# Kernel tuning notes

Measured on AMD Instinct MI355X. Metric: run time of the kernel, lower is better.

Reference implementation:

```python
import jax, jax.numpy as jnp
import numpy as np
from jax import lax

B, S, T = 16, 256, 800
V, D, M, H = 256, 512, 80, 1024
NH = 4; HD = D // NH; EH = 256  # encoder LSTM hidden per direction


def setup_inputs() -> dict:
    key = jax.random.key(0)
    it = iter(jax.random.split(key, 40))
    def rn(shape, s=0.05):
        return jax.random.normal(next(it), shape, jnp.float32) * s
    return dict(
        text_inputs=jax.random.randint(next(it), (B, S), 0, V),
        mel_targets=jax.random.normal(next(it), (B, T, M), jnp.float32),
        emb=rn((V, D), 0.1),
        conv_w=rn((3, D, D, 5)), conv_b=rn((3, D)),
        bn_gamma=jnp.ones((3, D)), bn_beta=jnp.zeros((3, D)),
        bn_mean=rn((3, D)), bn_var=jnp.ones((3, D)),
        enc_Wih_f=rn((4 * EH, D)), enc_Whh_f=rn((4 * EH, EH)), enc_b_f=rn((4 * EH,)),
        enc_Wih_b=rn((4 * EH, D)), enc_Whh_b=rn((4 * EH, EH)), enc_b_b=rn((4 * EH,)),
        Wq=rn((D, M)), bq=rn((D,)), Wk=rn((D, D)), bk=rn((D,)),
        Wv=rn((D, D)), bv=rn((D,)), Wo=rn((D, D)), bo=rn((D,)),
        dec_Wih1=rn((4 * H, D + M)), dec_b1=rn((4 * H,)),
        dec_Wih2=rn((4 * H, H)), dec_b2=rn((4 * H,)),
        mel_W=rn((M, H)), mel_b=rn((M,)),
        stop_W=rn((1, H)), stop_b=rn((1,)),
    )


def _lstm_cell_zero(x, Wih, b):
    # single-step LSTM cell from zero (h, c); original resets state every timestep
    g = x @ Wih.T + b
    i, f, gg, o = jnp.split(g, 4, axis=-1)
    c = jax.nn.sigmoid(i) * jnp.tanh(gg)  # c0 = 0 -> forget gate contributes nothing
    return jax.nn.sigmoid(o) * jnp.tanh(c)


def _lstm_scan(xs, Wih, Whh, b, hdim, reverse):
    # xs: (S, B, in); PyTorch gate order i,f,g,o
    def step(carry, xt):
        h, c = carry
        g = xt @ Wih.T + h @ Whh.T + b
        i, f, gg, o = jnp.split(g, 4, axis=-1)
        c = jax.nn.sigmoid(f) * c + jax.nn.sigmoid(i) * jnp.tanh(gg)
        h = jax.nn.sigmoid(o) * jnp.tanh(c)
        return (h, c), h
    z = jnp.zeros((xs.shape[1], hdim), xs.dtype)
    _, hs = lax.scan(step, (z, z), xs, reverse=reverse)
    return hs


def reference(text_inputs, mel_targets, emb, conv_w, conv_b, bn_gamma, bn_beta, bn_mean, bn_var, enc_Wih_f, enc_Whh_f, enc_b_f, enc_Wih_b, enc_Whh_b, enc_b_b, Wq, bq, Wk, bk, Wv, bv, Wo, bo, dec_Wih1, dec_b1, dec_Wih2, dec_b2, mel_W, mel_b, stop_W, stop_b):
    b_, t_, m_ = mel_targets.shape
    # ---- encoder ----
    x = emb[text_inputs].transpose(0, 2, 1)  # (B, D, S)
    for i in range(conv_w.shape[0]):
        x = lax.conv_general_dilated(x, conv_w[i], (1,), [(2, 2)], dimension_numbers=('NCH', 'OIH', 'NCH')) + conv_b[i][None, :, None]
        x = bn_gamma[i][None, :, None] * (x - bn_mean[i][None, :, None]) * lax.rsqrt(bn_var[i][None, :, None] + 1e-5) + bn_beta[i][None, :, None]
        x = jax.nn.relu(x)  # dropout in eval mode -> identity
    xs = x.transpose(2, 0, 1)  # (S, B, D)
    hf = _lstm_scan(xs, enc_Wih_f, enc_Whh_f, enc_b_f, EH, False)
    hb = _lstm_scan(xs, enc_Wih_b, enc_Whh_b, enc_b_b, EH, True)
    enc = jnp.concatenate([hf, hb], -1).transpose(1, 0, 2)  # (B, S, D)
    # ---- decoder (teacher forcing): per-step query = previous mel frame ----
    dec_in = jnp.concatenate([jnp.zeros((b_, 1, m_), mel_targets.dtype), mel_targets[:, :-1]], axis=1)  # (B, T, M)
    q = (dec_in @ Wq.T + bq).reshape(b_, t_, NH, HD)
    k = (enc @ Wk.T + bk).reshape(b_, -1, NH, HD)
    v = (enc @ Wv.T + bv).reshape(b_, -1, NH, HD)
    scores = jnp.einsum('bqhd,bkhd->bhqk', q, k) * (1.0 / np.sqrt(HD)).astype(np.float32)
    attn = jax.nn.softmax(scores, axis=-1)
    ctx = jnp.einsum('bhqk,bkhd->bqhd', attn, v).reshape(b_, t_, D) @ Wo.T + bo
    xcat = jnp.concatenate([ctx, dec_in], axis=-1)  # (B, T, D+M)
    # original re-inits decoder LSTM state each timestep -> stateless per-step cells
    h1 = _lstm_cell_zero(xcat, dec_Wih1, dec_b1)
    h2 = _lstm_cell_zero(h1, dec_Wih2, dec_b2)
    mel = h2 @ mel_W.T + mel_b      # (B, T, 80)
    stop = h2 @ stop_W.T + stop_b   # (B, T, 1) - logits (no sigmoid in training path)
    return mel, stop
```

## Files before the change

### kernel.cpp

```cpp
#include <hip/hip_runtime.h>
#include <hip/hip_bf16.h>
#include <math.h>

#define B_ 16
#define S_ 256
#define T_ 800
#define V_ 256
#define D_ 512
#define M_ 80
#define H_ 1024
#define NH_ 4
#define HD_ 128
#define EH_ 256

using bf16x8 = __attribute__((ext_vector_type(8))) short;
using f32x4  = __attribute__((ext_vector_type(4))) float;
typedef _Float16 half8 __attribute__((ext_vector_type(8)));

__device__ __forceinline__ float sigf(float x) { return 1.f / (1.f + __expf(-x)); }
__device__ __forceinline__ float tanhfast(float x) {
    float e = __expf(2.f * x);
    return 1.f - 2.f / (e + 1.f);
}

__device__ __forceinline__ unsigned short f2bf(float f) {
    unsigned int u = __float_as_uint(f);
    unsigned int r = (u + 0x7FFFu + ((u >> 16) & 1u)) >> 16;
    return (unsigned short)r;
}
__device__ __forceinline__ float bf2f(unsigned short u) {
    return __uint_as_float(((unsigned int)u) << 16);
}
__device__ __forceinline__ unsigned short h2u(_Float16 x) {
    union { _Float16 f; unsigned short u; } c; c.f = x; return c.u;
}

__device__ __forceinline__ void gl_lds16(const unsigned short* g, unsigned short* l) {
    __builtin_amdgcn_global_load_lds((const __attribute__((address_space(1))) void*)g,
                                     (__attribute__((address_space(3))) void*)l, 16, 0, 0);
}

__global__ __launch_bounds__(256) void gemm_mfma(
    const unsigned short* __restrict__ A, const unsigned short* __restrict__ Bw,
    void* __restrict__ Cv, const float* __restrict__ bias,
    int M, int N, int K, int ldc, int epi, int aperm,
    const float* __restrict__ cb)
{
    __shared__ unsigned short As[4096];
    __shared__ unsigned short Bs[4096];
    const int tid = threadIdx.x, w = tid >> 6, lane = tid & 63;
    const int bm = blockIdx.y * 128, bn = blockIdx.x * 128;
    const int wr = w >> 1, wc = w & 1;

    f32x4 acc[4][4];
#pragma unroll
    for (int m = 0; m < 4; ++m)
#pragma unroll
        for (int n = 0; n < 4; ++n) acc[m][n] = (f32x4){0.f, 0.f, 0.f, 0.f};

    const int r0 = w * 16 + (lane >> 2);
    const int k8 = (lane & 3) * 8;
    int ar0 = bm + r0, ar1 = bm + r0 + 64;
    if (aperm) {
        ar0 = ((ar0 & 15) << 8) | (ar0 >> 4);
        ar1 = ((ar1 & 15) << 8) | (ar1 >> 4);
    }
    const unsigned short* Ag0 = A + (size_t)ar0 * K + k8;
    const unsigned short* Ag1 = A + (size_t)ar1 * K + k8;
    const unsigned short* Bg = Bw + (size_t)(bn + r0) * K + k8;
    unsigned short* Al = As + w * 512;
    unsigned short* Bl = Bs + w * 512;

    for (int k0 = 0; k0 < K; k0 += 32) {
        __syncthreads();
        gl_lds16(Ag0 + k0, Al);
        gl_lds16(Ag1 + k0, Al + 2048);
        gl_lds16(Bg + k0, Bl);
        gl_lds16(Bg + (size_t)64 * K + k0, Bl + 2048);
        __syncthreads();
        bf16x8 a[4], b[4];
#pragma unroll
        for (int m = 0; m < 4; ++m)
            a[m] = *(const bf16x8*)(As + (wr * 64 + m * 16 + (lane & 15)) * 32 + (lane >> 4) * 8);
#pragma unroll
        for (int n = 0; n < 4; ++n)
            b[n] = *(const bf16x8*)(Bs + (wc * 64 + n * 16 + (lane & 15)) * 32 + (lane >> 4) * 8);
#pragma unroll
        for (int m = 0; m < 4; ++m)
#pragma unroll
            for (int n = 0; n < 4; ++n)
                acc[m][n] = __builtin_amdgcn_mfma_f32_16x16x32_bf16(a[m], b[n], acc[m][n], 0, 0, 0);
    }

    const int cr = (lane >> 4) * 4, ccol = lane & 15;
#pragma unroll
    for (int m = 0; m < 4; ++m)
#pragma unroll
        for (int n = 0; n < 4; ++n) {
            const int col = bn + wc * 64 + n * 16 + ccol;
            float bv;
            if (epi == 5)      bv = (col < 512) ? bias[col] : cb[col - 512];
            else if (epi == 4) bv = (col < 80) ? bias[col] : (col == 80 ? cb[0] : 0.f);
            else               bv = bias ? bias[col] : 0.f;
#pragma unroll
            for (int j = 0; j < 4; ++j) {
                const int row = bm + wr * 64 + m * 16 + cr + j;
                float v = acc[m][n][j] + bv;
                if (epi == 2) {
                    ((unsigned short*)Cv)[(size_t)row * ldc + col] = f2bf(v);
                } else if (epi == 5) {
                    if (col < 512) {
                        ((unsigned short*)Cv)[(size_t)row * 512 + col] = f2bf(v);
                    } else {
                        unsigned short* vTo = (unsigned short*)Cv + 2097152;
                        const int c2 = col - 512, hh = c2 >> 7, dd = c2 & 127;
                        const int bb2 = row >> 8, ss = row & 255;
                        vTo[((size_t)(bb2 * 4 + hh) * 128 + dd) * 256 + ss] = f2bf(v);
                    }
                } else if (epi == 4) {
                    if (col < 80)       ((float*)Cv)[(size_t)row * ldc + col] = v;
                    else if (col == 80) ((float*)Cv)[1024000 + row] = v;
                } else {
                    ((float*)Cv)[(size_t)row * ldc + col] = v;
                }
            }
        }
}

__global__ __launch_bounds__(256) void conv_mfma(
    const unsigned short* __restrict__ xin, const unsigned short* __restrict__ Bw,
    unsigned short* __restrict__ xout,
    const float* __restrict__ cb, const float* __restrict__ gam,
    const float* __restrict__ bet, const float* __restrict__ mu,
    const float* __restrict__ va, const unsigned short* __restrict__ zbuf)
{
    __shared__ unsigned short As[4096];
    __shared__ unsigned short Bs[4096];
    const int tid = threadIdx.x, w = tid >> 6, lane = tid & 63;
    const int bm = blockIdx.y * 128, bn = blockIdx.x * 128;
    const int wr = w >> 1, wc = w & 1;

    f32x4 acc[4][4];
#pragma unroll
    for (int m = 0; m < 4; ++m)
#pragma unroll
        for (int n = 0; n < 4; ++n) acc[m][n] = (f32x4){0.f, 0.f, 0.f, 0.f};

    const int r0 = w * 16 + (lane >> 2);
    const int k8 = (lane & 3) * 8;
    const int gr0 = bm + r0, gr1 = bm + r0 + 64;
    const int b0 = gr0 >> 8, s0 = gr0 & 255;
    const int b1 = gr1 >> 8, s1 = gr1 & 255;
    const unsigned short* Bg = Bw + (size_t)(bn + r0) * 2560 + k8;
    unsigned short* Al = As + w * 512;
    unsigned short* Bl = Bs + w * 512;

    for (int k0 = 0; k0 < 2560; k0 += 32) {
        const int kk = k0 >> 9;
        const int d0 = k0 & 511;
        const int s2a = s0 + kk - 2;
        const int s2b = s1 + kk - 2;
        const unsigned short* pa = (s2a >= 0 && s2a < 256)
            ? xin + ((size_t)(b0 * 256 + s2a) * 512 + d0 + k8) : zbuf;
        const unsigned short* pb = (s2b >= 0 && s2b < 256)
            ? xin + ((size_t)(b1 * 256 + s2b) * 512 + d0 + k8) : zbuf;
        __syncthreads();
        gl_lds16(pa, Al);
        gl_lds16(pb, Al + 2048);
        gl_lds16(Bg + k0, Bl);
        gl_lds16(Bg + (size_t)64 * 2560 + k0, Bl + 2048);
        __syncthreads();
        bf16x8 a[4], b[4];
#pragma unroll
        for (int m = 0; m < 4; ++m)
            a[m] = *(const bf16x8*)(As + (wr * 64 + m * 16 + (lane & 15)) * 32 + (lane >> 4) * 8);
#pragma unroll
        for (int n = 0; n < 4; ++n)
            b[n] = *(const bf16x8*)(Bs + (wc * 64 + n * 16 + (lane & 15)) * 32 + (lane >> 4) * 8);
#pragma unroll
        for (int m = 0; m < 4; ++m)
#pragma unroll
            for (int n = 0; n < 4; ++n)
                acc[m][n] = __builtin_amdgcn_mfma_f32_16x16x32_bf16(a[m], b[n], acc[m][n], 0, 0, 0);
    }

    const int cr = (lane >> 4) * 4, ccol = lane & 15;
#pragma unroll
    for (int m = 0; m < 4; ++m)
#pragma unroll
        for (int n = 0; n < 4; ++n) {
            const int col = bn + wc * 64 + n * 16 + ccol;
            const float bc = cb[col], gm = gam[col], bt = bet[col];
            const float mv = mu[col], iv = rsqrtf(va[col] + 1e-5f);
#pragma unroll
            for (int j = 0; j < 4; ++j) {
                const int row = bm + wr * 64 + m * 16 + cr + j;
                float x = acc[m][n][j] + bc;
                float y = fmaxf(0.f, gm * (x - mv) * iv + bt);
                xout[(size_t)row * 512 + col] = f2bf(y);
            }
        }
}

__global__ __launch_bounds__(256) void attn_qksm(
    const unsigned short* __restrict__ q, const unsigned short* __restrict__ k,
    unsigned short* __restrict__ probs)
{
    __shared__ unsigned short As[2048];
    __shared__ unsigned short Bs[8192];
    __shared__ float redm[64][4];
    __shared__ float reds[64][4];
    const int tid = threadIdx.x, wid = tid >> 6, lane = tid & 63;
    const int l15 = lane & 15, bq = lane >> 4;
    const int bm = blockIdx.x * 64;
    const int z = blockIdx.y, b = z >> 2, h = z & 3;

    const unsigned short* A  = q + ((size_t)b * T_) * 512 + h * 128;
    const unsigned short* Bw = k + ((size_t)b * S_) * 512 + h * 128;

    f32x4 acc[4][4];
#pragma unroll
    for (int m = 0; m < 4; ++m)
#pragma unroll
        for (int n = 0; n < 4; ++n) acc[m][n] = (f32x4){0.f, 0.f, 0.f, 0.f};

    const int r0 = wid * 16 + (lane >> 2);
    const int k8 = (lane & 3) * 8;

    for (int k0 = 0; k0 < 128; k0 += 32) {
        __syncthreads();
        gl_lds16(A + (size_t)(bm + r0) * 512 + k0 + k8, As + wid * 512);
        gl_lds16(Bw + (size_t)r0 * 512 + k0 + k8,          Bs + wid * 512);
        gl_lds16(Bw + (size_t)(64 + r0) * 512 + k0 + k8,   Bs + 2048 + wid * 512);
        gl_lds16(Bw + (size_t)(128 + r0) * 512 + k0 + k8,  Bs + 4096 + wid * 512);
        gl_lds16(Bw + (size_t)(192 + r0) * 512 + k0 + k8,  Bs + 6144 + wid * 512);
        __syncthreads();
        bf16x8 a[4], bb[4];
#pragma unroll
        for (int m = 0; m < 4; ++m)
            a[m] = *(const bf16x8*)(As + (m * 16 + l15) * 32 + bq * 8);
#pragma unroll
        for (int n = 0; n < 4; ++n)
            bb[n] = *(const bf16x8*)(Bs + (wid * 64 + n * 16 + l15) * 32 + bq * 8);
#pragma unroll
        for (int m = 0; m < 4; ++m)
#pragma unroll
            for (int n = 0; n < 4; ++n)
                acc[m][n] = __builtin_amdgcn_mfma_f32_16x16x32_bf16(a[m], bb[n], acc[m][n], 0, 0, 0);
    }

    const int cr = (lane >> 4) * 4, ccol = lane & 15;
    const float SC = 0.08838834764831843f;

#pragma unroll
    for (int m = 0; m < 4; ++m)
#pragma unroll
        for (int j = 0; j < 4; ++j) {
            float v = fmaxf(fmaxf(acc[m][0][j], acc[m][1][j]),
                            fmaxf(acc[m][2][j], acc[m][3][j]));
#pragma unroll
            for (int off = 1; off < 16; off <<= 1) v = fmaxf(v, __shfl_xor(v, off));
            if (ccol == 0) redm[m * 16 + cr + j][wid] = v;
        }
    __syncthreads();
#pragma unroll
    for (int m = 0; m < 4; ++m)
#pragma unroll
        for (int j = 0; j < 4; ++j) {
            const int r = m * 16 + cr + j;
            float mx = fmaxf(fmaxf(redm[r][0], redm[r][1]), fmaxf(redm[r][2], redm[r][3]));
            float s = 0.f;
#pragma unroll
            for (int n = 0; n < 4; ++n) {
                float p = __expf((acc[m][n][j] - mx) * SC);
                acc[m][n][j] = p;
                s += p;
            }
#pragma unroll
            for (int off = 1; off < 16; off <<= 1) s += __shfl_xor(s, off);
            if (ccol == 0) reds[r][wid] = s;
        }
    __syncthreads();
#pragma unroll
    for (int m = 0; m < 4; ++m)
#pragma unroll
        for (int j = 0; j < 4; ++j) {
            const int r = m * 16 + cr + j;
            const int row = bm + r;
            if (row >= T_) continue;
            const float inv = 1.f / (reds[r][0] + reds[r][1] + reds[r][2] + reds[r][3]);
#pragma unroll
            for (int n = 0; n < 4; ++n)
                probs[((size_t)z * T_ + row) * 256 + wid * 64 + n * 16 + ccol] =
                    f2bf(acc[m][n][j] * inv);
        }
}

__global__ __launch_bounds__(256) void attn_pv(
    const unsigned short* __restrict__ probs, const unsigned short* __restrict__ vT,
    unsigned short* __restrict__ ctx)
{
    __shared__ unsigned short As[4096];
    __shared__ unsigned short Bs[4096];
    const int tid = threadIdx.x, w = tid >> 6, lane = tid & 63;
    const int bm = blockIdx.y * 128;
    const int z = blockIdx.z, b = z >> 2, h = z & 3;
    const int wr = w >> 1, wc = w & 1;

    const unsigned short* A  = probs + (size_t)z * T_ * 256;
    const unsigned short* Bw = vT + (size_t)z * 128 * 256;

    f32x4 acc[4][4];
#pragma unroll
    for (int m = 0; m < 4; ++m)
#pragma unroll
        for (int n = 0; n < 4; ++n) acc[m][n] = (f32x4){0.f, 0.f, 0.f, 0.f};

    const int r0 = w * 16 + (lane >> 2);
    const int k8 = (lane & 3) * 8;
    const unsigned short* Ag = A + (size_t)(bm + r0) * 256 + k8;
    const unsigned short* Bg = Bw + (size_t)r0 * 256 + k8;
    unsigned short* Al = As + w * 512;
    unsigned short* Bl = Bs + w * 512;

    for (int k0 = 0; k0 < 256; k0 += 32) {
        __syncthreads();
        gl_lds16(Ag + k0, Al);
        gl_lds16(Ag + (size_t)64 * 256 + k0, Al + 2048);
        gl_lds16(Bg + k0, Bl);
        gl_lds16(Bg + (size_t)64 * 256 + k0, Bl + 2048);
        __syncthreads();
        bf16x8 a[4], bfr[4];
#pragma unroll
        for (int m = 0; m < 4; ++m)
            a[m] = *(const bf16x8*)(As + (wr * 64 + m * 16 + (lane & 15)) * 32 + (lane >> 4) * 8);
#pragma unroll
        for (int n = 0; n < 4; ++n)
            bfr[n] = *(const bf16x8*)(Bs + (wc * 64 + n * 16 + (lane & 15)) * 32 + (lane >> 4) * 8);
#pragma unroll
        for (int m = 0; m < 4; ++m)
#pragma unroll
            for (int n = 0; n < 4; ++n)
                acc[m][n] = __builtin_amdgcn_mfma_f32_16x16x32_bf16(a[m], bfr[n], acc[m][n], 0, 0, 0);
    }

    const int cr = (lane >> 4) * 4, ccol = lane & 15;
#pragma unroll
    for (int m = 0; m < 4; ++m)
#pragma unroll
        for (int n = 0; n < 4; ++n) {
            const int col = wc * 64 + n * 16 + ccol;
#pragma unroll
            for (int j = 0; j < 4; ++j) {
                const int row = bm + wr * 64 + m * 16 + cr + j;
                if (row < T_)
                    ctx[((size_t)b * T_ + row) * 512 + h * 128 + col] = f2bf(acc[m][n][j]);
            }
        }
}

__global__ void hist2enc(const _Float16* __restrict__ hist, unsigned short* __restrict__ enc)
{
    int idx = blockIdx.x * 256 + threadIdx.x;
    if (idx >= B_ * S_ * D_) return;
    int d = idx & 511;
    int bs = idx >> 9;
    int b = bs >> 8, s = bs & 255;
    int dir = d >> 8, hid = d & 255;
    enc[idx] = f2bf((float)hist[(((size_t)(dir * 16 + b) * 256 + s) * 256) + hid]);
}

__global__ void cvt_all(
    const float* __restrict__ conv_w, const float* __restrict__ Wih_f,
    const float* __restrict__ Wih_b, const float* __restrict__ Wk,
    const float* __restrict__ Wv, const float* __restrict__ Wq,
    const float* __restrict__ Wo, const float* __restrict__ Wih1,
    const float* __restrict__ Wih2, const float* __restrict__ melW,
    const float* __restrict__ stopW,
    const int* __restrict__ txt, const float* __restrict__ emb,
    const float* __restrict__ mel,
    unsigned short* __restrict__ cWc, unsigned short* __restrict__ cWif,
    unsigned short* __restrict__ cWib, unsigned short* __restrict__ cWkv,
    unsigned short* __restrict__ cWq, unsigned short* __restrict__ cWo,
    unsigned short* __restrict__ cW1, unsigned short* __restrict__ cW2,
    unsigned short* __restrict__ cWm,
    unsigned short* __restrict__ xb0, unsigned short* __restrict__ din,
    unsigned short* __restrict__ xcat)
{
    int idx = blockIdx.x * 256 + threadIdx.x;
    if (idx < 3932160) {
        int n = idx / 2560, c = idx - n * 2560;
        int kk = c >> 9, din2 = c & 511;
        cWc[idx] = f2bf(conv_w[(size_t)n * 2560 + din2 * 5 + kk]);
        return;
    }
    idx -= 3932160;
    if (idx < 524288) { cWif[idx] = f2bf(Wih_f[idx]); return; }
    idx -= 524288;
    if (idx < 524288) { cWib[idx] = f2bf(Wih_b[idx]); return; }
    idx -= 524288;
    if (idx < 524288) {
        int r = idx >> 9, k = idx & 511;
        cWkv[idx] = (r < 512) ? f2bf(Wk[(size_t)r * 512 + k])
                              : f2bf(Wv[(size_t)(r - 512) * 512 + k]);
        return;
    }
    idx -= 524288;
    if (idx < 49152) {
        int r = idx / 96, k = idx - r * 96;
        cWq[idx] = (k < 80) ? f2bf(Wq[(size_t)r * 80 + k]) : 0;
        return;
    }
    idx -= 49152;
    if (idx < 262144) { cWo[idx] = f2bf(Wo[idx]); return; }
    idx -= 262144;
    if (idx < 1867776) {
        int n = idx / 608, k = idx - n * 608;
        int orig = (n < 1024) ? n : n + 1024;
        cW1[idx] = (k < 592) ? f2bf(Wih1[(size_t)orig * 592 + k]) : 0;
        return;
    }
    idx -= 1867776;
    if (idx < 3145728) {
        int n = idx >> 10, k = idx & 1023;
        int orig = (n < 1024) ? n : n + 1024;
        cW2[idx] = f2bf(Wih2[(size_t)orig * 1024 + k]);
        return;
    }
    idx -= 3145728;
    if (idx < 131072) {
        int r = idx >> 10, k = idx & 1023;
        cWm[idx] = (r < 80) ? f2bf(melW[(size_t)r * 1024 + k])
                            : (r == 80 ? f2bf(stopW[k]) : 0);
        return;
    }
    idx -= 131072;
    if (idx < B_ * S_ * D_) {
        int bs = idx >> 9, dd = idx & 511;
        xb0[idx] = f2bf(emb[(size_t)txt[bs] * D_ + dd]);
        return;
    }
    idx -= B_ * S_ * D_;
    if (idx < B_ * T_ * 96) {
        int r = idx / 96, j = idx - r * 96;
        int b = r / T_, t = r - b * T_;
        float v = (j < M_ && t > 0) ? mel[((size_t)b * T_ + t - 1) * M_ + j] : 0.f;
        unsigned short bv = f2bf(v);
        din[(size_t)r * 96 + j] = bv;
        xcat[(size_t)r * 608 + 512 + j] = bv;
        return;
    }
}

__global__ void dec_cellb2(const unsigned short* __restrict__ g, const float* __restrict__ b,
                           unsigned short* __restrict__ h, int rows)
{
    int idx = blockIdx.x * 256 + threadIdx.x;
    if (idx >= rows * 512) return;
    int r = idx >> 9, j2 = (idx & 511) * 2;
    const unsigned short* gr = g + (size_t)r * 3072;
    ushort2 vi = *(const ushort2*)(gr + j2);
    ushort2 vg = *(const ushort2*)(gr + 1024 + j2);
    ushort2 vo = *(const ushort2*)(gr + 2048 + j2);
    float i0 = sigf(bf2f(vi.x) + b[j2]),          i1 = sigf(bf2f(vi.y) + b[j2 + 1]);
    float g0 = tanhfast(bf2f(vg.x) + b[2048 + j2]), g1 = tanhfast(bf2f(vg.y) + b[2048 + j2 + 1]);
    float o0 = sigf(bf2f(vo.x) + b[3072 + j2]),   o1 = sigf(bf2f(vo.y) + b[3072 + j2 + 1]);
    ushort2 o;
    o.x = f2bf(o0 * tanhfast(i0 * g0));
    o.y = f2bf(o1 * tanhfast(i1 * g1));
    *(ushort2*)(h + (size_t)r * 1024 + j2) = o;
}

__global__ __launch_bounds__(1024, 4) void lstm_persist9(
    const float* __restrict__ gi_f, const float* __restrict__ gi_b,
    const float* __restrict__ Wf, const float* __restrict__ Wb,
    _Float16* __restrict__ hist,
    unsigned long long* __restrict__ hstage)
{
    const int blk = blockIdx.x;
    const int dir = blk >> 1, half = blk & 1;
    const float* gi = dir ? gi_b : gi_f;
    const float* W  = dir ? Wb : Wf;
    const int tid = threadIdx.x, wid = tid >> 6, lane = tid & 63;
    const int l15 = lane & 15, q = lane >> 4;
    const int half4 = half * 4, ph4 = (half ^ 1) * 4;

    __shared__ _Float16 h_lds[16][264];
    __shared__ float exch[512][17];

    half8 wOA[4], wPA[4], wOB[4], wPB[4];
    {
        const int gt0 = wid >> 3, hb0 = wid & 7;
        const int gt1 = (wid + 16) >> 3;
        const float* wr0 = W + (size_t)(gt0 * 256 + half * 128 + hb0 * 16 + l15) * 256;
        const float* wr1 = W + (size_t)(gt1 * 256 + half * 128 + hb0 * 16 + l15) * 256;
#pragma unroll
        for (int i = 0; i < 4; ++i) {
            const int kO = (half4 + i) * 32 + q * 8;
            const int kP = (ph4 + i) * 32 + q * 8;
            half8 a, b, c, d;
#pragma unroll
            for (int j = 0; j < 8; ++j) {
                a[j] = (_Float16)wr0[kO + j];
                b[j] = (_Float16)wr0[kP + j];
                c[j] = (_Float16)wr1[kO + j];
                d[j] = (_Float16)wr1[kP + j];
            }
            wOA[i] = a; wPA[i] = b; wOB[i] = c; wPB[i] = d;
        }
    }
    for (int i = tid; i < 16 * 264; i += 1024) ((_Float16*)h_lds)[i] = (_Float16)0.f;
    for (int i = tid; i < 512 * 17; i += 1024) ((float*)exch)[i] = 0.f;

    const int hid = tid & 127;
    const int ba  = tid >> 7;
    const int bb  = ba + 8;
    const int gh  = half * 128 + hid;
    const int pc  = (half ^ 1) * 128 + hid;
    float c0 = 0.f, c1 = 0.f;

    const int exr0 = (wid >> 3) * 128 + (wid & 7) * 16 + l15;
    const int exr1 = ((wid + 16) >> 3) * 128 + (wid & 7) * 16 + l15;

    const int own_base = ((dir * 2 + half) * 8 + ba) * 128 + hid;
    const int par_base = ((dir * 2 + (half ^ 1)) * 8 + ba) * 128 + hid;

    float gp0[4], gp1[4];
    {
        const int s0 = dir ? 255 : 0;
        const float* g0 = gi + ((size_t)s0 * 16 + ba) * 1024 + gh;
        const float* g1 = gi + ((size_t)s0 * 16 + bb) * 1024 + gh;
#pragma unroll
        for (int g2 = 0; g2 < 4; ++g2) { gp0[g2] = g0[g2 * 256]; gp1[g2] = g1[g2 * 256]; }
    }
    __syncthreads();

    for (int step = 0; step < 256; ++step) {
        const int s = dir ? (255 - step) : step;
        const unsigned int tag = (unsigned int)(step + 1);
        const int slot = (step & 1) * 4096;

        float h0, h1;
        {
            float xi = exch[hid][ba] + gp0[0];
            float xf = exch[128 + hid][ba] + gp0[1];
            float xg = exch[256 + hid][ba] + gp0[2];
            float xo = exch[384 + hid][ba] + gp0[3];
            float ig = sigf(xi), fg = sigf(xf), gg = tanhfast(xg), og = sigf(xo);
            c0 = fg * c0 + ig * gg; h0 = og * tanhfast(c0);
            xi = exch[hid][bb] + gp1[0];
            xf = exch[128 + hid][bb] + gp1[1];
            xg = exch[256 + hid][bb] + gp1[2];
            xo = exch[384 + hid][bb] + gp1[3];
            ig = sigf(xi); fg = sigf(xf); gg = tanhfast(xg); og = sigf(xo);
            c1 = fg * c1 + ig * gg; h1 = og * tanhfast(c1);
        }
        {
            unsigned int d32 = (unsigned int)h2u((_Float16)h0) |
                               ((unsigned int)h2u((_Float16)h1) << 16);
            unsigned long long wv = ((unsigned long long)tag << 32) | d32;
            __hip_atomic_store(&hstage[slot + own_base], wv,
                               __ATOMIC_RELAXED, __HIP_MEMORY_SCOPE_AGENT);
        }
        h_lds[ba][gh] = (_Float16)h0;
        h_lds[bb][gh] = (_Float16)h1;
        hist[(((size_t)(dir * 16 + ba) * 256 + s) * 256) + gh] = (_Float16)h0;
        hist[(((size_t)(dir * 16 + bb) * 256 + s) * 256) + gh] = (_Float16)h1;
        if (step < 255) {
            const int s2 = dir ? (254 - step) : (step + 1);
            const float* g0 = gi + ((size_t)s2 * 16 + ba) * 1024 + gh;
            const float* g1 = gi + ((size_t)s2 * 16 + bb) * 1024 + gh;
#pragma unroll
            for (int g2 = 0; g2 < 4; ++g2) { gp0[g2] = g0[g2 * 256]; gp1[g2] = g1[g2 * 256]; }
        }
        __syncthreads();

        if (step < 255) {
            f32x4 acc0 = (f32x4){0.f, 0.f, 0.f, 0.f};
            f32x4 acc1 = (f32x4){0.f, 0.f, 0.f, 0.f};
            const _Float16* hrow = &h_lds[l15][0];
#pragma unroll
            for (int i = 0; i < 4; ++i) {
                half8 a = *(const half8*)(hrow + (half4 + i) * 32 + q * 8);
                acc0 = __builtin_amdgcn_mfma_f32_16x16x32_f16(a, wOA[i], acc0, 0, 0, 0);
                acc1 = __builtin_amdgcn_mfma_f32_16x16x32_f16(a, wOB[i], acc1, 0, 0, 0);
            }
            {
                unsigned long long pv;
                do {
                    pv = __hip_atomic_load(&hstage[slot + par_base],
                                           __ATOMIC_RELAXED, __HIP_MEMORY_SCOPE_AGENT);
                } while ((unsigned int)(pv >> 32) != tag);
                unsigned int d32 = (unsigned int)pv;
                *(unsigned short*)&h_lds[ba][pc] = (unsigned short)(d32 & 0xFFFF);
                *(unsigned short*)&h_lds[bb][pc] = (unsigned short)(d32 >> 16);
            }
            __syncthreads();
#pragma unroll
            for (int i = 0; i < 4; ++i) {
                half8 a = *(const half8*)(hrow + (ph4 + i) * 32 + q * 8);
                acc0 = __builtin_amdgcn_mfma_f32_16x16x32_f16(a, wPA[i], acc0, 0, 0, 0);
                acc1 = __builtin_amdgcn_mfma_f32_16x16x32_f16(a, wPB[i], acc1, 0, 0, 0);
            }
            *(f32x4*)&exch[exr0][q * 4] = acc0;
            *(f32x4*)&exch[exr1][q * 4] = acc1;
            __syncthreads();
        }
    }
}

static inline void launch_mfma(hipStream_t st, const unsigned short* A, const unsigned short* B,
                               void* C, const float* bias, int M, int N, int K, int ldc,
                               int epi = 0, int aperm = 0, const float* cb = nullptr)
{
    dim3 grid(N / 128, M / 128);
    gemm_mfma<<<grid, 256, 0, st>>>(A, B, C, bias, M, N, K, ldc, epi, aperm, cb);
}

extern "C" void kernel_launch(void* const* d_in, const int* in_sizes, int n_in,
                              void* d_out, int out_size, void* d_ws, size_t ws_size,
                              hipStream_t stream)
{
    const int*   text   = (const int*)d_in[0];
    const float* mel_t  = (const float*)d_in[1];
    const float* emb    = (const float*)d_in[2];
    const float* conv_w = (const float*)d_in[3];
    const float* conv_b = (const float*)d_in[4];
    const float* bn_g   = (const float*)d_in[5];
    const float* bn_b   = (const float*)d_in[6];
    const float* bn_m   = (const float*)d_in[7];
    const float* bn_v   = (const float*)d_in[8];
    const float* Wih_f  = (const float*)d_in[9];
    const float* Whh_f  = (const float*)d_in[10];
    const float* b_f    = (const float*)d_in[11];
    const float* Wih_b  = (const float*)d_in[12];
    const float* Whh_b  = (const float*)d_in[13];
    const float* b_b    = (const float*)d_in[14];
    const float* Wq     = (const float*)d_in[15];
    const float* bq     = (const float*)d_in[16];
    const float* Wk     = (const float*)d_in[17];
    const float* bk     = (const float*)d_in[18];
    const float* Wv     = (const float*)d_in[19];
    const float* bv     = (const float*)d_in[20];
    const float* Wo     = (const float*)d_in[21];
    const float* bo     = (const float*)d_in[22];
    const float* Wih1   = (const float*)d_in[23];
    const float* b1     = (const float*)d_in[24];
    const float* Wih2   = (const float*)d_in[25];
    const float* b2     = (const float*)d_in[26];
    const float* melW   = (const float*)d_in[27];
    const float* melb   = (const float*)d_in[28];
    const float* stopW  = (const float*)d_in[29];
    const float* stopb  = (const float*)d_in[30];
    float* out = (float*)d_out;
    (void)in_sizes; (void)n_in; (void)out_size; (void)ws_size;

    float* ws = (float*)d_ws;
    float* big  = ws;
    float* pool = ws + 13107200;

    unsigned long long* hstage = (unsigned long long*)(ws + 6000000);
    const unsigned short* zbuf = (const unsigned short*)(hstage + 8192);

    float*          gi_f   = pool + 0;
    float*          gi_b   = pool + 4194304;
    unsigned short* enc_bf = (unsigned short*)(pool + 8388608);
    unsigned short* xb0    = (unsigned short*)(pool + 9437184);
    unsigned short* xb1    = (unsigned short*)(pool + 10485760);
    unsigned short* xb2    = (unsigned short*)(pool + 11534336);
    unsigned short* xb3    = (unsigned short*)(pool + 12582912);
    _Float16*       hist   = (_Float16*)(pool + 14155776);
    unsigned short* kbf    = (unsigned short*)(pool + 0);
    unsigned short* vT     = (unsigned short*)(pool + 1048576);
    unsigned short* qbf    = (unsigned short*)(pool + 2097152);
    unsigned short* probs  = (unsigned short*)(pool + 9437184);
    unsigned short* dinb   = (unsigned short*)(pool + 16008192);
    unsigned short* ctxb   = (unsigned short*)(pool + 16622592);
    unsigned short* gatesb = (unsigned short*)(pool + 0);
    unsigned short* h2b    = (unsigned short*)big;
    unsigned short* h1b    = (unsigned short*)(big + 4000000);
    unsigned short* xcat   = (unsigned short*)(pool + 19899392);
    float*          WB     = pool + 23790592;
    unsigned short* cWc  = (unsigned short*)(WB + 0);
    unsigned short* cWif = (unsigned short*)(WB + 1966080);
    unsigned short* cWib = (unsigned short*)(WB + 2228224);
    unsigned short* cWkv = (unsigned short*)(WB + 2490368);
    unsigned short* cWq  = (unsigned short*)(WB + 2752512);
    unsigned short* cWo  = (unsigned short*)(WB + 2777088);
    unsigned short* cW1  = (unsigned short*)(WB + 2908160);
    unsigned short* cW2  = (unsigned short*)(WB + 3842048);
    unsigned short* cWm  = (unsigned short*)(WB + 5414912);

    auto ceil256 = [](int n) { return (n + 255) / 256; };

    hipMemsetAsync(hstage, 0, 8192 * 8 + 128, stream);

    cvt_all<<<ceil256(10960896 + B_ * S_ * D_ + B_ * T_ * 96), 256, 0, stream>>>(
        conv_w, Wih_f, Wih_b, Wk, Wv, Wq, Wo, Wih1, Wih2, melW, stopW,
        text, emb, mel_t,
        cWc, cWif, cWib, cWkv, cWq, cWo, cW1, cW2, cWm,
        xb0, dinb, xcat);

    {
        dim3 grid(4, 32);
        conv_mfma<<<grid, 256, 0, stream>>>(xb0, cWc,               xb1,
            conv_b, bn_g, bn_b, bn_m, bn_v, zbuf);
        conv_mfma<<<grid, 256, 0, stream>>>(xb1, cWc + 1310720,     xb2,
            conv_b + 512, bn_g + 512, bn_b + 512, bn_m + 512, bn_v + 512, zbuf);
        conv_mfma<<<grid, 256, 0, stream>>>(xb2, cWc + 2621440,     xb3,
            conv_b + 1024, bn_g + 1024, bn_b + 1024, bn_m + 1024, bn_v + 1024, zbuf);
    }

    launch_mfma(stream, xb3, cWif, gi_f, b_f, S_ * B_, 1024, 512, 1024, 0, 1);
    launch_mfma(stream, xb3, cWib, gi_b, b_b, S_ * B_, 1024, 512, 1024, 0, 1);
    lstm_persist9<<<4, 1024, 0, stream>>>(gi_f, gi_b, Whh_f, Whh_b, hist, hstage);
    hist2enc<<<ceil256(B_ * S_ * D_), 256, 0, stream>>>(hist, enc_bf);

    launch_mfma(stream, enc_bf, cWkv, kbf, bk, B_ * S_, 1024, 512, 512, 5, 0, bv);
    launch_mfma(stream, dinb, cWq, qbf, bq, B_ * T_, 512, 96, 512, 2);

    attn_qksm<<<dim3(13, 64), 256, 0, stream>>>(qbf, kbf, probs);
    attn_pv<<<dim3(1, 7, 64), 256, 0, stream>>>(probs, vT, ctxb);

    launch_mfma(stream, ctxb, cWo, xcat, bo, B_ * T_, 512, 512, 608, 2);

    launch_mfma(stream, xcat, cW1, gatesb, nullptr, B_ * T_, 3072, 608, 3072, 2);
    dec_cellb2<<<ceil256(B_ * T_ * 512), 256, 0, stream>>>(gatesb, b1, h1b, B_ * T_);
    launch_mfma(stream, h1b, cW2, gatesb, nullptr, B_ * T_, 3072, 1024, 3072, 2);
    dec_cellb2<<<ceil256(B_ * T_ * 512), 256, 0, stream>>>(gatesb, b2, h2b, B_ * T_);

    launch_mfma(stream, h2b, cWm, out, melb, B_ * T_, 128, 1024, 80, 4, 0, stopb);
}
```

Baseline: 1.333 ms.

## Merge encoder input GEMMs, read LSTM history directly, swizzle decoder GEMM blocks

The forward and backward encoder input projections become one N=2048 GEMM with a split-bias epilogue, and the LSTM reads its gates with a 2048 stride. The LSTM now writes its history in bf16, and the K/V GEMM reads it through a strided A-addressing mode, which removes the hist2enc conversion kernel. A workgroup-ID swizzle is added to the two large decoder gate GEMMs to improve L2 reuse. In exchange, the LSTM history loses fp16 precision for bf16, and the addressing logic becomes more complex.

```diff
diff --git a/kernel.cpp b/kernel.cpp
--- a/kernel.cpp
+++ b/kernel.cpp
@@ -43,13 +43,20 @@
 __global__ __launch_bounds__(256) void gemm_mfma(
     const unsigned short* __restrict__ A, const unsigned short* __restrict__ Bw,
     void* __restrict__ Cv, const float* __restrict__ bias,
-    int M, int N, int K, int ldc, int epi, int aperm,
+    int M, int N, int K, int ldc, int epi, int aperm, int swz,
     const float* __restrict__ cb)
 {
     __shared__ unsigned short As[4096];
     __shared__ unsigned short Bs[4096];
     const int tid = threadIdx.x, w = tid >> 6, lane = tid & 63;
-    const int bm = blockIdx.y * 128, bn = blockIdx.x * 128;
+    int bx = blockIdx.x, by = blockIdx.y;
+    if (swz) {
+        const int nwg = gridDim.x * gridDim.y;
+        const int id = by * gridDim.x + bx;
+        const int nid = (id & 7) * (nwg >> 3) + (id >> 3);
+        bx = nid % gridDim.x; by = nid / gridDim.x;
+    }
+    const int bm = by * 128, bn = bx * 128;
     const int wr = w >> 1, wc = w & 1;
 
     f32x4 acc[4][4];
@@ -61,20 +68,22 @@
     const int r0 = w * 16 + (lane >> 2);
     const int k8 = (lane & 3) * 8;
     int ar0 = bm + r0, ar1 = bm + r0 + 64;
-    if (aperm) {
+    if (aperm == 1) {
         ar0 = ((ar0 & 15) << 8) | (ar0 >> 4);
         ar1 = ((ar1 & 15) << 8) | (ar1 >> 4);
     }
-    const unsigned short* Ag0 = A + (size_t)ar0 * K + k8;
-    const unsigned short* Ag1 = A + (size_t)ar1 * K + k8;
+    const size_t astr = (aperm == 2) ? 256 : (size_t)K;
+    const unsigned short* Ag0 = A + (size_t)ar0 * astr + k8;
+    const unsigned short* Ag1 = A + (size_t)ar1 * astr + k8;
     const unsigned short* Bg = Bw + (size_t)(bn + r0) * K + k8;
     unsigned short* Al = As + w * 512;
     unsigned short* Bl = Bs + w * 512;
 
     for (int k0 = 0; k0 < K; k0 += 32) {
-        __syncthreads();
-        gl_lds16(Ag0 + k0, Al);
-        gl_lds16(Ag1 + k0, Al + 2048);
+        const int kA = (aperm == 2) ? ((k0 & 255) + ((k0 >> 8) << 20)) : k0;
+        __syncthreads();
+        gl_lds16(Ag0 + kA, Al);
+        gl_lds16(Ag1 + kA, Al + 2048);
         gl_lds16(Bg + k0, Bl);
         gl_lds16(Bg + (size_t)64 * K + k0, Bl + 2048);
         __syncthreads();
@@ -100,6 +109,7 @@
             const int col = bn + wc * 64 + n * 16 + ccol;
             float bv;
             if (epi == 5)      bv = (col < 512) ? bias[col] : cb[col - 512];
+            else if (epi == 6) bv = (col < 1024) ? bias[col] : cb[col - 1024];
             else if (epi == 4) bv = (col < 80) ? bias[col] : (col == 80 ? cb[0] : 0.f);
             else               bv = bias ? bias[col] : 0.f;
 #pragma unroll
@@ -359,17 +369,6 @@
         }
 }
 
-__global__ void hist2enc(const _Float16* __restrict__ hist, unsigned short* __restrict__ enc)
-{
-    int idx = blockIdx.x * 256 + threadIdx.x;
-    if (idx >= B_ * S_ * D_) return;
-    int d = idx & 511;
-    int bs = idx >> 9;
-    int b = bs >> 8, s = bs & 255;
-    int dir = d >> 8, hid = d & 255;
-    enc[idx] = f2bf((float)hist[(((size_t)(dir * 16 + b) * 256 + s) * 256) + hid]);
-}
-
 __global__ void cvt_all(
     const float* __restrict__ conv_w, const float* __restrict__ Wih_f,
     const float* __restrict__ Wih_b, const float* __restrict__ Wk,
@@ -474,7 +473,7 @@
 __global__ __launch_bounds__(1024, 4) void lstm_persist9(
     const float* __restrict__ gi_f, const float* __restrict__ gi_b,
     const float* __restrict__ Wf, const float* __restrict__ Wb,
-    _Float16* __restrict__ hist,
+    unsigned short* __restrict__ hist,
     unsigned long long* __restrict__ hstage)
 {
     const int blk = blockIdx.x;
@@ -528,8 +527,8 @@
     float gp0[4], gp1[4];
     {
         const int s0 = dir ? 255 : 0;
-        const float* g0 = gi + ((size_t)s0 * 16 + ba) * 1024 + gh;
-        const float* g1 = gi + ((size_t)s0 * 16 + bb) * 1024 + gh;
+        const float* g0 = gi + ((size_t)s0 * 16 + ba) * 2048 + gh;
+        const float* g1 = gi + ((size_t)s0 * 16 + bb) * 2048 + gh;
 #pragma unroll
         for (int g2 = 0; g2 < 4; ++g2) { gp0[g2] = g0[g2 * 256]; gp1[g2] = g1[g2 * 256]; }
     }
@@ -564,12 +563,12 @@
         }
         h_lds[ba][gh] = (_Float16)h0;
         h_lds[bb][gh] = (_Float16)h1;
-        hist[(((size_t)(dir * 16 + ba) * 256 + s) * 256) + gh] = (_Float16)h0;
-        hist[(((size_t)(dir * 16 + bb) * 256 + s) * 256) + gh] = (_Float16)h1;
+        hist[(((size_t)(dir * 16 + ba) * 256 + s) * 256) + gh] = f2bf(h0);
+        hist[(((size_t)(dir * 16 + bb) * 256 + s) * 256) + gh] = f2bf(h1);
         if (step < 255) {
             const int s2 = dir ? (254 - step) : (step + 1);
-            const float* g0 = gi + ((size_t)s2 * 16 + ba) * 1024 + gh;
-            const float* g1 = gi + ((size_t)s2 * 16 + bb) * 1024 + gh;
+            const float* g0 = gi + ((size_t)s2 * 16 + ba) * 2048 + gh;
+            const float* g1 = gi + ((size_t)s2 * 16 + bb) * 2048 + gh;
 #pragma unroll
             for (int g2 = 0; g2 < 4; ++g2) { gp0[g2] = g0[g2 * 256]; gp1[g2] = g1[g2 * 256]; }
         }
@@ -611,10 +610,11 @@
 
 static inline void launch_mfma(hipStream_t st, const unsigned short* A, const unsigned short* B,
                                void* C, const float* bias, int M, int N, int K, int ldc,
-                               int epi = 0, int aperm = 0, const float* cb = nullptr)
+                               int epi = 0, int aperm = 0, const float* cb = nullptr,
+                               int swz = 0)
 {
     dim3 grid(N / 128, M / 128);
-    gemm_mfma<<<grid, 256, 0, st>>>(A, B, C, bias, M, N, K, ldc, epi, aperm, cb);
+    gemm_mfma<<<grid, 256, 0, st>>>(A, B, C, bias, M, N, K, ldc, epi, aperm, swz, cb);
 }
 
 extern "C" void kernel_launch(void* const* d_in, const int* in_sizes, int n_in,
@@ -662,14 +662,14 @@
     unsigned long long* hstage = (unsigned long long*)(ws + 6000000);
     const unsigned short* zbuf = (const unsigned short*)(hstage + 8192);
 
-    float*          gi_f   = pool + 0;
-    float*          gi_b   = pool + 4194304;
-    unsigned short* enc_bf = (unsigned short*)(pool + 8388608);
+    float*          gibuf  = pool + 0;
+    float*          gi_f   = gibuf;
+    float*          gi_b   = gibuf + 1024;
     unsigned short* xb0    = (unsigned short*)(pool + 9437184);
     unsigned short* xb1    = (unsigned short*)(pool + 10485760);
     unsigned short* xb2    = (unsigned short*)(pool + 11534336);
     unsigned short* xb3    = (unsigned short*)(pool + 12582912);
-    _Float16*       hist   = (_Float16*)(pool + 14155776);
+    unsigned short* hist   = (unsigned short*)(pool + 14155776);
     unsigned short* kbf    = (unsigned short*)(pool + 0);
     unsigned short* vT     = (unsigned short*)(pool + 1048576);
     unsigned short* qbf    = (unsigned short*)(pool + 2097152);
@@ -703,20 +703,18 @@
 
     {
         dim3 grid(4, 32);
-        conv_mfma<<<grid, 256, 0, stream>>>(xb0, cWc,               xb1,
+        conv_mfma<<<grid, 256, 0, stream>>>(xb0, cWc,           xb1,
             conv_b, bn_g, bn_b, bn_m, bn_v, zbuf);
-        conv_mfma<<<grid, 256, 0, stream>>>(xb1, cWc + 1310720,     xb2,
+        conv_mfma<<<grid, 256, 0, stream>>>(xb1, cWc + 1310720, xb2,
             conv_b + 512, bn_g + 512, bn_b + 512, bn_m + 512, bn_v + 512, zbuf);
-        conv_mfma<<<grid, 256, 0, stream>>>(xb2, cWc + 2621440,     xb3,
+        conv_mfma<<<grid, 256, 0, stream>>>(xb2, cWc + 2621440, xb3,
             conv_b + 1024, bn_g + 1024, bn_b + 1024, bn_m + 1024, bn_v + 1024, zbuf);
     }
 
-    launch_mfma(stream, xb3, cWif, gi_f, b_f, S_ * B_, 1024, 512, 1024, 0, 1);
-    launch_mfma(stream, xb3, cWib, gi_b, b_b, S_ * B_, 1024, 512, 1024, 0, 1);
+    launch_mfma(stream, xb3, cWif, gibuf, b_f, S_ * B_, 2048, 512, 2048, 6, 1, b_b);
     lstm_persist9<<<4, 1024, 0, stream>>>(gi_f, gi_b, Whh_f, Whh_b, hist, hstage);
-    hist2enc<<<ceil256(B_ * S_ * D_), 256, 0, stream>>>(hist, enc_bf);
-
-    launch_mfma(stream, enc_bf, cWkv, kbf, bk, B_ * S_, 1024, 512, 512, 5, 0, bv);
+
+    launch_mfma(stream, hist, cWkv, kbf, bk, B_ * S_, 1024, 512, 512, 5, 2, bv);
     launch_mfma(stream, dinb, cWq, qbf, bq, B_ * T_, 512, 96, 512, 2);
 
     attn_qksm<<<dim3(13, 64), 256, 0, stream>>>(qbf, kbf, probs);
@@ -724,9 +722,9 @@
 
     launch_mfma(stream, ctxb, cWo, xcat, bo, B_ * T_, 512, 512, 608, 2);
 
-    launch_mfma(stream, xcat, cW1, gatesb, nullptr, B_ * T_, 3072, 608, 3072, 2);
+    launch_mfma(stream, xcat, cW1, gatesb, nullptr, B_ * T_, 3072, 608, 3072, 2, 0, nullptr, 1);
     dec_cellb2<<<ceil256(B_ * T_ * 512), 256, 0, stream>>>(gatesb, b1, h1b, B_ * T_);
-    launch_mfma(stream, h1b, cW2, gatesb, nullptr, B_ * T_, 3072, 1024, 3072, 2);
+    launch_mfma(stream, h1b, cW2, gatesb, nullptr, B_ * T_, 3072, 1024, 3072, 2, 0, nullptr, 1);
     dec_cellb2<<<ceil256(B_ * T_ * 512), 256, 0, stream>>>(gatesb, b2, h2b, B_ * T_);
 
     launch_mfma(stream, h2b, cWm, out, melb, B_ * T_, 128, 1024, 80, 4, 0, stopb);
```

Result: no change. 1.332 ms (-0.1%).
